# Kernel tuning notes

Measured on AMD Instinct MI355X. Metric: run time of the kernel, lower is better.

## Reference

```python
import jax, jax.numpy as jnp
import numpy as np

NUM_INPUTS = 784
NUM_OUTPUTS = 784
WIDTH_POW = 10
WIDTH = 2 ** WIDTH_POW          # 1024
HALF = WIDTH // 2               # 512
DEPTH = 8
BDEPTH = 10
DEGREE = 2
BATCH = 4096

# knots from the source: tensor([-256..256]) / 32
_KNOTS = np.array([-256., -128., -64., -32., -16., -8., -4., -2., -1., 0.,
                   1., 2., 4., 8., 16., 32., 64., 128., 256.], dtype=np.float32) / 32.0
# clamped (open) knot vector: repeat endpoints `degree` times
_T = np.concatenate([np.full(DEGREE, _KNOTS[0]), _KNOTS, np.full(DEGREE, _KNOTS[-1])]).astype(np.float32)
SPLINE_DIM = len(_T) - DEGREE - 1  # 20 basis functions


def _bspline_basis(x):
    """Cox-de Boor B-spline basis, vectorized over all elements of x.
    Returns basis of shape x.shape + (SPLINE_DIM,)."""
    t = jnp.asarray(_T)
    x = jnp.clip(x, _T[0], _T[-1] - 1e-6)  # clamp to knot span (eval domain)
    xe = x[..., None]
    B = ((xe >= t[:-1]) & (xe < t[1:])).astype(x.dtype)  # degree-0 indicators
    for k in range(1, DEGREE + 1):
        tj, tjk = t[:-(k + 1)], t[k:-1]
        tj1, tjk1 = t[1:-k], t[k + 1:]
        d1, d2 = tjk - tj, tjk1 - tj1
        w1 = jnp.where(d1 > 0, (xe - tj) / jnp.where(d1 > 0, d1, 1.0), 0.0)
        w2 = jnp.where(d2 > 0, (tjk1 - xe) / jnp.where(d2 > 0, d2, 1.0), 0.0)
        B = w1 * B[..., :-1] + w2 * B[..., 1:]
    return B  # [..., SPLINE_DIM]


def _butterfly(X, params):
    """OrthogonalButterfly.forward. params: [HALF, BDEPTH]. X: [B, WIDTH]."""
    Bsz = X.shape[0]
    for d in range(BDEPTH):
        theta = params[:, d]
        c, s = jnp.cos(theta), jnp.sin(theta)
        X0, X1 = X[:, :HALF], X[:, HALF:]
        n0 = X0 * c + X1 * s
        n1 = -X0 * s + X1 * c
        # perm[i] = i//2 (even) / i//2 + half (odd) == interleave halves
        X = jnp.stack([n0, n1], axis=2).reshape(Bsz, WIDTH)
    return X


def _forward(X, butterfly_params, spline_coefs):
    Bsz = X.shape[0]
    X = jnp.concatenate([X, jnp.zeros((Bsz, WIDTH - NUM_INPUTS), X.dtype)], axis=1)
    for i in range(DEPTH):
        X = _butterfly(X, butterfly_params[i])
        if i != DEPTH - 1:
            # ReversibleActivation: X0 += spline(X1), per-column spline coefs
            X0, X1 = X[:, :HALF], X[:, HALF:]
            act = jnp.einsum('bwd,wd->bw', _bspline_basis(X1), spline_coefs[i])
            X = jnp.concatenate([X0 + act, X1], axis=1)
    return X[:, :NUM_OUTPUTS]


def setup_inputs() -> dict:
    key = jax.random.key(0)
    k1, k2, k3 = jax.random.split(key, 3)
    X = jax.random.normal(k1, (BATCH, NUM_INPUTS), dtype=jnp.float32)
    butterfly_params = jax.random.uniform(k2, (DEPTH, HALF, BDEPTH), dtype=jnp.float32) * (2.0 * np.pi)
    spline_coefs = jax.random.uniform(k3, (DEPTH - 1, HALF, SPLINE_DIM), dtype=jnp.float32) * 0.2 - 0.1
    return {"X": X, "butterfly_params": butterfly_params, "spline_coefs": spline_coefs}


def reference(X, butterfly_params, spline_coefs):
    return _forward(X, butterfly_params, spline_coefs)
```

## Files before the change

### kernel.cpp

```cpp
#include <hip/hip_runtime.h>

#define NIN 784
#define WIDTH 1024
#define HALF 512
#define DEPTH 8
#define BDEPTH 10
#define BATCH 4096
#define SPLINE_DIM 20
#define NQ 18
#define LSTRIDE 8192

typedef __attribute__((ext_vector_type(2))) float f32x2;

__device__ float d_T[23] = {
  -8.f, -8.f, -8.f, -4.f, -2.f, -1.f, -0.5f, -0.25f, -0.125f, -0.0625f,
  -0.03125f, 0.f, 0.03125f, 0.0625f, 0.125f, 0.25f, 0.5f, 1.f, 2.f, 4.f,
  8.f, 8.f, 8.f };

__global__ void prep_kernel(const float* __restrict__ bp,
                            const float* __restrict__ sc,
                            float2* __restrict__ cs,
                            float4* __restrict__ qt) {
  int gid = blockIdx.x * 256 + threadIdx.x;
  if (gid < DEPTH * BDEPTH * 1024) {
    int slot = gid & 1023;
    int d = (gid >> 10) % BDEPTH;
    int i = gid / (BDEPTH * 1024);
    int n = 0;
#pragma unroll
    for (int b = 0; b < 10; ++b) {
      int src = b - d; if (src < 0) src += 10;
      n |= ((slot >> src) & 1) << b;
    }
    int pj = n & 511;
    float theta = bp[(i * HALF + pj) * BDEPTH + d];
    float c = cosf(theta), s = sinf(theta);
    float2 val = make_float2(c, (n & 512) ? -s : s);
    long base = (long)i * LSTRIDE;
    if (d < 4) {
      int r = slot >> 6, lane = slot & 63;
      int mr = 8 >> d;
      if ((r & mr) == 0) {
        int q;
        if (d == 0)      q = r;
        else if (d == 1) q = (r & 3) | ((r >> 3) << 2);
        else if (d == 2) q = ((r >> 2) << 1) | (r & 1);
        else             q = r >> 1;
        int tbl = d >> 1, sub = d & 1;
        cs[base + tbl * 1024 + (q * 64 + lane) * 2 + sub] = val;
      }
    } else {
      int p = (d - 4) >> 1, sub = (d - 4) & 1;
      cs[base + 2048 + p * 2048 + slot * 2 + sub] = val;
    }
  }
  int gid2 = gid - DEPTH * BDEPTH * 1024;
  if (gid2 >= 0 && gid2 < (DEPTH - 1) * NQ * HALF) {
    int w = gid2 & 511;
    int mi = (gid2 >> 9) % NQ;
    int i = gid2 / (NQ * HALF);
    int m = mi + 2;
    const float* cf = sc + (i * HALF + w) * SPLINE_DIM;
    double c0 = cf[mi], c1 = cf[mi + 1], c2 = cf[mi + 2];
    double tm1 = d_T[m - 1], tm = d_T[m], tp1 = d_T[m + 1], tp2 = d_T[m + 2];
    double h = tp1 - tm;
    double us[3] = { 0.0, 0.5 * h, 0.75 * h };
    double y[3];
#pragma unroll
    for (int k = 0; k < 3; ++k) {
      double x = tm + us[k];
      double left1 = x - tm, right1 = tp1 - x, left2 = x - tm1, right2 = tp2 - x;
      double inv1 = 1.0 / (tp1 - tm);
      double N0 = right1 * inv1, N1 = left1 * inv1;
      double temp0 = N0 / (tp1 - tm1);
      double B0 = right1 * temp0;
      double saved = left2 * temp0;
      double temp1 = N1 / (tp2 - tm);
      double B1 = right2 * temp1 + saved;
      double B2 = left1 * temp1;
      y[k] = c0 * B0 + c1 * B1 + c2 * B2;
    }
    double d1 = y[1] - y[0], d2 = y[2] - y[0];
    double u1 = us[1], u2 = us[2];
    double det = u1 * u2 * (u2 - u1);
    double Bq = (d1 * u2 * u2 - d2 * u1 * u1) / det;
    double Cq = (d2 * u1 - d1 * u2) / det;
    qt[gid2] = make_float4((float)y[0], (float)Bq, (float)Cq, (float)tm);
  }
}

template <int M>
__device__ __forceinline__ float shfx(float x, int lane) {
  if constexpr (M == 1)
    return __int_as_float(__builtin_amdgcn_mov_dpp(__float_as_int(x), 0xB1, 0xF, 0xF, true));
  else if constexpr (M == 2)
    return __int_as_float(__builtin_amdgcn_mov_dpp(__float_as_int(x), 0x4E, 0xF, 0xF, true));
  else if constexpr (M == 4)
    return __int_as_float(__builtin_amdgcn_ds_swizzle(__float_as_int(x), 0x101F));
  else if constexpr (M == 8)
    return __int_as_float(__builtin_amdgcn_mov_dpp(__float_as_int(x), 0x128, 0xF, 0xF, true));
  else if constexpr (M == 16) {
#if __has_builtin(__builtin_amdgcn_permlane16_swap)
    auto pr = __builtin_amdgcn_permlane16_swap(__float_as_uint(x), __float_as_uint(x), false, false);
    return __uint_as_float((lane & 16) ? pr[0] : pr[1]);
#else
    return __int_as_float(__builtin_amdgcn_ds_swizzle(__float_as_int(x), 0x401F));
#endif
  } else {
#if __has_builtin(__builtin_amdgcn_permlane32_swap)
    auto pr = __builtin_amdgcn_permlane32_swap(__float_as_uint(x), __float_as_uint(x), false, false);
    return __uint_as_float((lane & 32) ? pr[0] : pr[1]);
#else
    return __shfl_xor(x, 32, 64);
#endif
  }
}

__device__ __forceinline__ float qspline(float x, const float4* __restrict__ qL, int w) {
  x = fminf(fmaxf(x, -8.0f), 7.9999990f);
  float ax = fabsf(x);
  unsigned bits = __float_as_uint(ax);
  int e = (int)(bits >> 23) - 127;
  int ce = e + ((bits & 0x7fffffu) ? 1 : 0);
  int m = (x > 0.f) ? (17 + e) : (5 - ce);
  m = (ax < 0.03125f) ? ((x < 0.f) ? 10 : 11) : m;
  float4 qc = qL[(m - 2) * HALF + w];
  float u = x - qc.w;
  return fmaf(u, fmaf(u, qc.z, qc.y), qc.x);
}

typedef __attribute__((address_space(3))) unsigned int lds_u32;
typedef __attribute__((address_space(1))) const unsigned int glb_u32;

__device__ __forceinline__ void stage_issue(const float2* __restrict__ src,
                                            float2* dst, int wv) {
#pragma unroll
  for (int k = 0; k < 16; ++k) {
    int seg = k * 4 + wv;
    const char* g = (const char*)src + seg * 1024 + (threadIdx.x & 63) * 16;
    char* l = (char*)dst + seg * 1024;
    __builtin_amdgcn_global_load_lds((glb_u32*)g, (lds_u32*)l, 16, 0, 0);
  }
}

#define PK_MUL_BH(d, a, b)                                                    \
  asm("v_pk_mul_f32 %0, %1, %2 op_sel:[0,1] op_sel_hi:[1,1]"                  \
      : "=v"(d) : "v"(a), "v"(b))
#define PK_FMA_BL(d, a, b, c)                                                 \
  asm("v_pk_fma_f32 %0, %1, %2, %3 op_sel:[0,0,0] op_sel_hi:[1,0,1]"          \
      : "=v"(d) : "v"(a), "v"(b), "v"(c))
#define PK_FMA_BL_NC(d, a, b, c)                                              \
  asm("v_pk_fma_f32 %0, %1, %2, %3 op_sel:[0,0,0] op_sel_hi:[1,0,1] "         \
      "neg_lo:[0,0,1] neg_hi:[0,0,1]"                                         \
      : "=v"(d) : "v"(a), "v"(b), "v"(c))

union F4 { float4 f; f32x2 h[2]; };

#define ROT(rz, rp, csp) do {                                                 \
    f32x2 _t1, _t2;                                                           \
    PK_MUL_BH(_t1, st[rp], csp);                                     \
    PK_MUL_BH(_t2, st[rz], csp);                                     \
    PK_FMA_BL(st[rz], st[rz], csp, _t1);                       \
    PK_FMA_BL_NC(st[rp], st[rp], csp, _t2);                    \
  } while (0)

#define LSTEP1(r, M, csp) do {                                                \
    f32x2 _q = { shfx<M>(st[r].x, lane), shfx<M>(st[r].y, lane) };            \
    f32x2 _t;                                                                 \
    PK_MUL_BH(_t, _q, csp);                                                   \
    PK_FMA_BL(st[r], st[r], csp, _t);                                         \
  } while (0)

#define LPAIR(p, M1, M2) do {                                                 \
    const float4* _pp = (const float4*)(cur + 2048 + (p) * 2048);             \
    _Pragma("unroll") for (int r = 0; r < 16; ++r) {                          \
      F4 v; v.f = _pp[r * 64 + lane];                                         \
      LSTEP1(r, M1, v.h[0]);                                                  \
      LSTEP1(r, M2, v.h[1]);                                                  \
    }                                                                         \
  } while (0)

__global__ __launch_bounds__(256, 2) void fwd_kernel(
    const float* __restrict__ X, const float2* __restrict__ cs,
    const float4* __restrict__ qt, float* __restrict__ out) {
  __shared__ float2 buf[LSTRIDE];
  int tid = threadIdx.x;
  int lane = tid & 63;
  int wv = tid >> 6;
  int row0 = blockIdx.x * 8 + wv * 2;

  const float* x0p = X + (long)row0 * NIN;
  const float* x1p = X + (long)(row0 + 1) * NIN;
  f32x2 st[16];
#pragma unroll
  for (int r = 0; r < 16; ++r) {
    int w = r * 64 + lane;
    bool in = (w < NIN);
    st[r] = (f32x2){ in ? x0p[w] : 0.f, in ? x1p[w] : 0.f };
  }

#pragma unroll 1
  for (int i = 0; i < DEPTH; ++i) {
    const float2* cur = buf;

    __syncthreads();
    stage_issue(cs + (long)i * LSTRIDE, buf, wv);
    asm volatile("s_waitcnt vmcnt(0)" ::: "memory");
    __syncthreads();

    {
      const float4* cp = (const float4*)cur;
      F4 V[8];
#pragma unroll
      for (int q = 0; q < 8; ++q) V[q].f = cp[q * 64 + lane];
#pragma unroll
      for (int q = 0; q < 8; ++q) ROT(q, q + 8, V[q].h[0]);
#pragma unroll
      for (int q = 0; q < 8; ++q) {
        const int rz = (q < 4) ? q : q + 4;
        ROT(rz, rz + 4, V[q].h[1]);
      }
    }
    {
      const float4* cp = (const float4*)(cur + 1024);
      F4 V[8];
#pragma unroll
      for (int q = 0; q < 8; ++q) V[q].f = cp[q * 64 + lane];
#pragma unroll
      for (int q = 0; q < 8; ++q) {
        const int rz = ((q >> 1) << 2) | (q & 1);
        ROT(rz, rz + 2, V[q].h[0]);
      }
#pragma unroll
      for (int q = 0; q < 8; ++q) {
        const int rz = 2 * q;
        ROT(rz, rz + 1, V[q].h[1]);
      }
    }
    LPAIR(0, 32, 16);
    LPAIR(1, 8, 4);
    LPAIR(2, 2, 1);

    if (i != DEPTH - 1) {
      const float4* qL = qt + i * (NQ * HALF);
#pragma unroll
      for (int r = 8; r < 16; ++r) {
        int w = ((r - 8) << 6) | lane;
        st[r - 8].x += qspline(st[r].x, qL, w);
        st[r - 8].y += qspline(st[r].y, qL, w);
      }
    }
  }

  float* o0 = out + (long)row0 * NIN;
  float* o1 = out + (long)(row0 + 1) * NIN;
#pragma unroll
  for (int r = 0; r < 13; ++r) {
    int w = r * 64 + lane;
    if (w < NIN) { o0[w] = st[r].x; o1[w] = st[r].y; }
  }
}

extern "C" void kernel_launch(void* const* d_in, const int* in_sizes, int n_in,
                              void* d_out, int out_size, void* d_ws, size_t ws_size,
                              hipStream_t stream) {
  const float* X  = (const float*)d_in[0];
  const float* bp = (const float*)d_in[1];
  const float* sc = (const float*)d_in[2];
  float* out = (float*)d_out;

  float2* cs = (float2*)d_ws;
  float4* qt = (float4*)((char*)d_ws + DEPTH * LSTRIDE * sizeof(float2));

  int prep_threads = DEPTH * BDEPTH * 1024 + (DEPTH - 1) * NQ * HALF;
  prep_kernel<<<(prep_threads + 255) / 256, 256, 0, stream>>>(bp, sc, cs, qt);
  fwd_kernel<<<BATCH / 8, 256, 0, stream>>>(X, cs, qt, out);
}
```

Baseline: 59.62 us.

## Load rotation coefficients directly from global into registers, dropping LDS staging

```diff
diff --git a/kernel.cpp b/kernel.cpp
--- a/kernel.cpp
+++ b/kernel.cpp
@@ -129,20 +129,6 @@
   return fmaf(u, fmaf(u, qc.z, qc.y), qc.x);
 }
 
-typedef __attribute__((address_space(3))) unsigned int lds_u32;
-typedef __attribute__((address_space(1))) const unsigned int glb_u32;
-
-__device__ __forceinline__ void stage_issue(const float2* __restrict__ src,
-                                            float2* dst, int wv) {
-#pragma unroll
-  for (int k = 0; k < 16; ++k) {
-    int seg = k * 4 + wv;
-    const char* g = (const char*)src + seg * 1024 + (threadIdx.x & 63) * 16;
-    char* l = (char*)dst + seg * 1024;
-    __builtin_amdgcn_global_load_lds((glb_u32*)g, (lds_u32*)l, 16, 0, 0);
-  }
-}
-
 #define PK_MUL_BH(d, a, b)                                                    \
   asm("v_pk_mul_f32 %0, %1, %2 op_sel:[0,1] op_sel_hi:[1,1]"                  \
       : "=v"(d) : "v"(a), "v"(b))
@@ -171,19 +157,16 @@
     PK_FMA_BL(st[r], st[r], csp, _t);                                         \
   } while (0)
 
-#define LPAIR(p, M1, M2) do {                                                 \
-    const float4* _pp = (const float4*)(cur + 2048 + (p) * 2048);             \
+#define LPAIRR(T, M1, M2) do {                                                \
     _Pragma("unroll") for (int r = 0; r < 16; ++r) {                          \
-      F4 v; v.f = _pp[r * 64 + lane];                                         \
-      LSTEP1(r, M1, v.h[0]);                                                  \
-      LSTEP1(r, M2, v.h[1]);                                                  \
+      LSTEP1(r, M1, T[r].h[0]);                                               \
+      LSTEP1(r, M2, T[r].h[1]);                                               \
     }                                                                         \
   } while (0)
 
 __global__ __launch_bounds__(256, 2) void fwd_kernel(
     const float* __restrict__ X, const float2* __restrict__ cs,
     const float4* __restrict__ qt, float* __restrict__ out) {
-  __shared__ float2 buf[LSTRIDE];
   int tid = threadIdx.x;
   int lane = tid & 63;
   int wv = tid >> 6;
@@ -201,45 +184,45 @@
 
 #pragma unroll 1
   for (int i = 0; i < DEPTH; ++i) {
-    const float2* cur = buf;
-
-    __syncthreads();
-    stage_issue(cs + (long)i * LSTRIDE, buf, wv);
-    asm volatile("s_waitcnt vmcnt(0)" ::: "memory");
-    __syncthreads();
-
-    {
-      const float4* cp = (const float4*)cur;
-      F4 V[8];
-#pragma unroll
-      for (int q = 0; q < 8; ++q) V[q].f = cp[q * 64 + lane];
-#pragma unroll
-      for (int q = 0; q < 8; ++q) ROT(q, q + 8, V[q].h[0]);
-#pragma unroll
-      for (int q = 0; q < 8; ++q) {
-        const int rz = (q < 4) ? q : q + 4;
-        ROT(rz, rz + 4, V[q].h[1]);
-      }
-    }
-    {
-      const float4* cp = (const float4*)(cur + 1024);
-      F4 V[8];
-#pragma unroll
-      for (int q = 0; q < 8; ++q) V[q].f = cp[q * 64 + lane];
-#pragma unroll
-      for (int q = 0; q < 8; ++q) {
-        const int rz = ((q >> 1) << 2) | (q & 1);
-        ROT(rz, rz + 2, V[q].h[0]);
-      }
-#pragma unroll
-      for (int q = 0; q < 8; ++q) {
-        const int rz = 2 * q;
-        ROT(rz, rz + 1, V[q].h[1]);
-      }
-    }
-    LPAIR(0, 32, 16);
-    LPAIR(1, 8, 4);
-    LPAIR(2, 2, 1);
+    const float4* base = (const float4*)(cs + (long)i * LSTRIDE);
+
+    F4 V01[16], T0[16];
+#pragma unroll
+    for (int q = 0; q < 16; ++q) V01[q].f = base[q * 64 + lane];
+#pragma unroll
+    for (int r = 0; r < 16; ++r) T0[r].f = base[1024 + r * 64 + lane];
+    __builtin_amdgcn_sched_barrier(0);
+
+#pragma unroll
+    for (int q = 0; q < 8; ++q) ROT(q, q + 8, V01[q].h[0]);
+#pragma unroll
+    for (int q = 0; q < 8; ++q) {
+      const int rz = (q < 4) ? q : q + 4;
+      ROT(rz, rz + 4, V01[q].h[1]);
+    }
+#pragma unroll
+    for (int q = 0; q < 8; ++q) {
+      const int rz = ((q >> 1) << 2) | (q & 1);
+      ROT(rz, rz + 2, V01[8 + q].h[0]);
+    }
+#pragma unroll
+    for (int q = 0; q < 8; ++q) {
+      const int rz = 2 * q;
+      ROT(rz, rz + 1, V01[8 + q].h[1]);
+    }
+    F4 T1[16];
+#pragma unroll
+    for (int r = 0; r < 16; ++r) T1[r].f = base[2048 + r * 64 + lane];
+    __builtin_amdgcn_sched_barrier(0);
+
+    LPAIRR(T0, 32, 16);
+    F4 T2[16];
+#pragma unroll
+    for (int r = 0; r < 16; ++r) T2[r].f = base[3072 + r * 64 + lane];
+    __builtin_amdgcn_sched_barrier(0);
+
+    LPAIRR(T1, 8, 4);
+    LPAIRR(T2, 2, 1);
 
     if (i != DEPTH - 1) {
       const float4* qL = qt + i * (NQ * HALF);
```

After: 71.79 us. 20.4% more time.
